# Optimization experiments

Measured on AMD Instinct MI355X. Metric: run time of the kernel, lower is better.

The kernel has to match this reference:

```python
import jax, jax.numpy as jnp
import numpy as np

IN_F = 512
OUT_F = 512
ALPHA = 0.2   # LeakyReLU negative slope
NEG_INF = -9e15


def setup_inputs() -> dict:
    key = jax.random.key(0)
    k1, k2, k3, k4 = jax.random.split(key, 4)
    B, S = 8, 2048
    hidden_state = jax.random.normal(k1, (B, S, IN_F), dtype=jnp.float32)
    adjacent_matrix = jax.random.uniform(k2, (B, S, S), dtype=jnp.float32)
    # nn.Linear weight (no bias): stored as [out, in] in torch; we keep [in, out] for x @ W
    bound = 1.0 / np.sqrt(IN_F)
    W = jax.random.uniform(k3, (IN_F, OUT_F), dtype=jnp.float32, minval=-bound, maxval=bound)
    # xavier_uniform with gain=1.414 on a: shape [2*out, 1]
    a_bound = 1.414 * np.sqrt(6.0 / (2 * OUT_F + 1))
    a = jax.random.uniform(k4, (2 * OUT_F, 1), dtype=jnp.float32, minval=-a_bound, maxval=a_bound)
    return {"hidden_state": hidden_state, "adjacent_matrix": adjacent_matrix, "W": W, "a": a}


def reference(hidden_state, adjacent_matrix, W, a):
    # Wh: [B, S, out]
    Wh = jnp.einsum('bsi,io->bso', hidden_state, W)
    # additive attention: Wh1 + Wh2^T -> [B, S, S]
    Wh1 = Wh @ a[:OUT_F, :]            # [B, S, 1]
    Wh2 = Wh @ a[OUT_F:, :]            # [B, S, 1]
    e = Wh1 + jnp.swapaxes(Wh2, 1, 2)  # [B, S, S]
    e = jax.nn.leaky_relu(e, negative_slope=ALPHA)
    attention = jnp.where(adjacent_matrix > 0.5, e, NEG_INF)
    # NOTE: original softmaxes over dim=1 (the *row* index), faithfully reproduced
    attention = jax.nn.softmax(attention, axis=1)
    # dropout is identity at inference (training=False)
    h_prime = jnp.einsum('bst,bto->bso', attention, Wh)
    return jax.nn.elu(h_prime)  # concat=True path
```

## Files before the change

### kernel.cpp

```cpp
#include <hip/hip_runtime.h>
#include <hip/hip_bf16.h>
#include <stdint.h>

#define SDIM 2048
#define BDIM 8
#define FDIM 512
constexpr float ALPHA = 0.2f;

typedef __attribute__((ext_vector_type(8))) short bf16x8;
typedef __attribute__((ext_vector_type(4))) float f32x4;

__device__ __forceinline__ unsigned short f2bf(float x) {
  __hip_bfloat16 h = __float2bfloat16(x);
  return *reinterpret_cast<unsigned short*>(&h);
}

__device__ __forceinline__ void gload_lds16(const void* g, void* l) {
  __builtin_amdgcn_global_load_lds(
      (const __attribute__((address_space(1))) unsigned int*)(uintptr_t)g,
      (__attribute__((address_space(3))) unsigned int*)(uintptr_t)l,
      16, 0, 0);
}

__global__ void k0_prep(const float* __restrict__ W, const float* __restrict__ a,
                        float* __restrict__ wa, __hip_bfloat16* __restrict__ WT) {
  int i = blockIdx.x;
  int lane = threadIdx.x;
  float s1 = 0.f, s2 = 0.f;
  for (int o = lane; o < FDIM; o += 64) {
    float w = W[i * FDIM + o];
    s1 += w * a[o];
    s2 += w * a[FDIM + o];
    WT[o * FDIM + i] = __float2bfloat16(w);
  }
  #pragma unroll
  for (int off = 32; off > 0; off >>= 1) {
    s1 += __shfl_down(s1, off);
    s2 += __shfl_down(s2, off);
  }
  if (lane == 0) { wa[i] = s1; wa[FDIM + i] = s2; }
}

__global__ __launch_bounds__(256) void k1_rows(const float* __restrict__ H,
                                               const float* __restrict__ wa,
                                               float* __restrict__ Wh1, float* __restrict__ Wh2,
                                               __hip_bfloat16* __restrict__ Hb) {
  int wid = threadIdx.x >> 6, lane = threadIdx.x & 63;
  long r = (long)blockIdx.x * 4 + wid;
  const float* hr = H + r * FDIM;
  float4 v0 = ((const float4*)hr)[lane];
  float4 v1 = ((const float4*)hr)[lane + 64];
  float4 wa10 = ((const float4*)wa)[lane];
  float4 wa11 = ((const float4*)wa)[lane + 64];
  float4 wa20 = ((const float4*)(wa + FDIM))[lane];
  float4 wa21 = ((const float4*)(wa + FDIM))[lane + 64];
  float s1 = v0.x*wa10.x + v0.y*wa10.y + v0.z*wa10.z + v0.w*wa10.w
           + v1.x*wa11.x + v1.y*wa11.y + v1.z*wa11.z + v1.w*wa11.w;
  float s2 = v0.x*wa20.x + v0.y*wa20.y + v0.z*wa20.z + v0.w*wa20.w
           + v1.x*wa21.x + v1.y*wa21.y + v1.z*wa21.z + v1.w*wa21.w;
  ushort4 u0 = { f2bf(v0.x), f2bf(v0.y), f2bf(v0.z), f2bf(v0.w) };
  ushort4 u1 = { f2bf(v1.x), f2bf(v1.y), f2bf(v1.z), f2bf(v1.w) };
  ushort4* hb = (ushort4*)(Hb + r * FDIM);
  hb[lane] = u0;
  hb[lane + 64] = u1;
  #pragma unroll
  for (int off = 32; off > 0; off >>= 1) {
    s1 += __shfl_down(s1, off);
    s2 += __shfl_down(s2, off);
  }
  if (lane == 0) { Wh1[r] = s1; Wh2[r] = s2; }
}

__global__ __launch_bounds__(256) void k2_z(const float* __restrict__ adj,
                                            const float* __restrict__ Wh1,
                                            const float* __restrict__ Wh2,
                                            float* __restrict__ Zp,
                                            __hip_bfloat16* __restrict__ P) {
  int t = blockIdx.x * 256 + threadIdx.x;
  int b = blockIdx.y;
  int c = blockIdx.z;
  float w2 = Wh2[b * SDIM + t];
  const float* arow = adj + ((long)b * SDIM + c * 64) * SDIM + t;
  const float* w1p = Wh1 + b * SDIM + c * 64;
  __hip_bfloat16* prow = P + ((long)b * SDIM + c * 64) * SDIM + t;
  float z = 0.f;
  #pragma unroll 8
  for (int s = 0; s < 64; ++s) {
    float av = arow[(long)s * SDIM];
    float e = w1p[s] + w2;
    e = fmaxf(e, ALPHA * e);
    float p = (av > 0.5f) ? __expf(e) : 0.f;
    z += p;
    prow[(long)s * SDIM] = __float2bfloat16(p);
  }
  Zp[(b * 32 + c) * SDIM + t] = z;
}

__global__ __launch_bounds__(256) void k3_gemm(const __hip_bfloat16* __restrict__ WTm,
                                               const __hip_bfloat16* __restrict__ Hb,
                                               const float* __restrict__ Zp,
                                               __hip_bfloat16* __restrict__ VT) {
  __shared__ __align__(16) __hip_bfloat16 Asm[2][128 * 32];
  __shared__ __align__(16) __hip_bfloat16 Bsm[2][128 * 32];
  __shared__ float ztmp[256];
  __shared__ float rzLds[128];
  const int o0 = blockIdx.x * 128;
  const int t0 = blockIdx.y * 128;
  const int b = blockIdx.z;
  const int tid = threadIdx.x;
  const int w = tid >> 6, lane = tid & 63;
  const int wm = w >> 1, wn = w & 1;
  const int fr = lane & 15, fq = lane >> 4;
  const int lr = lane >> 2, lb = (lane & 3) * 16;

  const __hip_bfloat16* Abase = WTm + (long)o0 * FDIM;
  const __hip_bfloat16* Bbase = Hb + ((long)b * SDIM + t0) * FDIM;

  f32x4 acc[4][4] = {};

  auto stage = [&](int kk, int buf) {
    #pragma unroll
    for (int g = 0; g < 2; ++g) {
      int rbase = g * 64 + w * 16;
      int row = rbase + lr;
      gload_lds16((const char*)(Abase + (long)row * FDIM + kk * 32) + lb,
                  (char*)&Asm[buf][0] + rbase * 64);
      gload_lds16((const char*)(Bbase + (long)row * FDIM + kk * 32) + lb,
                  (char*)&Bsm[buf][0] + rbase * 64);
    }
  };

  stage(0, 0);
  {
    int tl = tid & 127, h = tid >> 7;
    int t = t0 + tl;
    float z = 0.f;
    #pragma unroll
    for (int c = 0; c < 16; ++c)
      z += Zp[((b * 32) + h * 16 + c) * SDIM + t];
    ztmp[tid] = z;
  }
  __syncthreads();
  if (tid < 128) rzLds[tid] = 1.0f / (ztmp[tid] + ztmp[tid + 128]);
  __syncthreads();

  for (int kk = 0; kk < 16; ++kk) {
    int cur = kk & 1;
    if (kk < 15) stage(kk + 1, cur ^ 1);
    bf16x8 af[4], bf_[4];
    #pragma unroll
    for (int mf = 0; mf < 4; ++mf)
      af[mf] = *(const bf16x8*)((const char*)&Asm[cur][0] + (wm * 64 + mf * 16 + fr) * 64 + fq * 16);
    #pragma unroll
    for (int nf = 0; nf < 4; ++nf)
      bf_[nf] = *(const bf16x8*)((const char*)&Bsm[cur][0] + (wn * 64 + nf * 16 + fr) * 64 + fq * 16);
    #pragma unroll
    for (int mf = 0; mf < 4; ++mf)
      #pragma unroll
      for (int nf = 0; nf < 4; ++nf)
        acc[mf][nf] = __builtin_amdgcn_mfma_f32_16x16x32_bf16(af[mf], bf_[nf], acc[mf][nf], 0, 0, 0);
    __syncthreads();
  }

  #pragma unroll
  for (int nf = 0; nf < 4; ++nf) {
    int tl = wn * 64 + nf * 16 + fr;
    int t = t0 + tl;
    float rz = rzLds[tl];
    #pragma unroll
    for (int mf = 0; mf < 4; ++mf) {
      #pragma unroll
      for (int r = 0; r < 4; ++r) {
        int o = o0 + wm * 64 + mf * 16 + fq * 4 + r;
        VT[((long)(b * FDIM + o)) * SDIM + t] = __float2bfloat16(acc[mf][nf][r] * rz);
      }
    }
  }
}

__global__ __launch_bounds__(256, 2) void k4_pv(const __hip_bfloat16* __restrict__ P,
                                                const __hip_bfloat16* __restrict__ VT,
                                                float* __restrict__ out) {
  __shared__ __align__(16) __hip_bfloat16 Vsm[3][256 * 32];
  __shared__ __align__(16) __hip_bfloat16 Psm[3][64 * 32];
  const int b  = blockIdx.x;
  const int s0 = blockIdx.y * 64;
  const int ob = blockIdx.z * 256;
  const int tid = threadIdx.x;
  const int w = tid >> 6, lane = tid & 63;
  const int fr = lane & 15, fq = lane >> 4;
  const int srow = lane >> 2;
  const int sgam = (lane & 3) ^ ((lane >> 2) & 3);

  const char* vtG = (const char*)(VT + ((long)(b * FDIM + ob)) * SDIM);
  const char* pG  = (const char*)(P + ((long)(b * SDIM + s0)) * SDIM);

  f32x4 acc[4][4] = {};

  auto stageV = [&](int p, int buf) {
    #pragma unroll
    for (int g = 0; g < 4; ++g) {
      int row = w * 64 + g * 16 + srow;
      gload_lds16(vtG + ((long)row * SDIM + p * 32 + sgam * 8) * 2,
                  (char*)&Vsm[0][0] + buf * 16384 + w * 4096 + g * 1024);
    }
  };
  auto stageP = [&](int p, int buf) {
    int row = w * 16 + srow;
    gload_lds16(pG + ((long)row * SDIM + p * 32 + sgam * 8) * 2,
                (char*)&Psm[0][0] + buf * 4096 + w * 1024);
  };

  stageV(0, 0); stageP(0, 0);
  stageV(1, 1); stageP(1, 1);
  asm volatile("s_waitcnt vmcnt(5)" ::: "memory");
  __builtin_amdgcn_sched_barrier(0);
  __builtin_amdgcn_s_barrier();

  int bufR = 0;
  int bufS = 2;
  for (int p = 0; p < 64; ++p) {
    if (p <= 61) { stageV(p + 2, bufS); stageP(p + 2, bufS); }
    __builtin_amdgcn_sched_barrier(0);

    bf16x8 pa[4], vb[4];
    #pragma unroll
    for (int mf = 0; mf < 4; ++mf)
      pa[mf] = *(const bf16x8*)((const char*)&Psm[0][0] + bufR * 4096 + mf * 1024
                                + fr * 64 + (fq ^ (fr & 3)) * 16);
    #pragma unroll
    for (int nf = 0; nf < 4; ++nf)
      vb[nf] = *(const bf16x8*)((const char*)&Vsm[0][0] + bufR * 16384 + w * 4096 + nf * 1024
                                + fr * 64 + (fq ^ (fr & 3)) * 16);
    __builtin_amdgcn_s_setprio(1);
    #pragma unroll
    for (int mf = 0; mf < 4; ++mf)
      #pragma unroll
      for (int nf = 0; nf < 4; ++nf)
        acc[mf][nf] = __builtin_amdgcn_mfma_f32_16x16x32_bf16(pa[mf], vb[nf], acc[mf][nf], 0, 0, 0);
    __builtin_amdgcn_s_setprio(0);

    if (p <= 61) { asm volatile("s_waitcnt vmcnt(5)" ::: "memory"); }
    else         { asm volatile("s_waitcnt vmcnt(0)" ::: "memory"); }
    asm volatile("s_waitcnt lgkmcnt(0)" ::: "memory");
    __builtin_amdgcn_sched_barrier(0);
    __builtin_amdgcn_s_barrier();

    bufR = (bufR == 2) ? 0 : bufR + 1;
    bufS = (bufS == 2) ? 0 : bufS + 1;
  }

  float* orow = out + ((long)b * SDIM + s0) * FDIM + ob + w * 64;
  #pragma unroll
  for (int mf = 0; mf < 4; ++mf) {
    #pragma unroll
    for (int nf = 0; nf < 4; ++nf) {
      #pragma unroll
      for (int r = 0; r < 4; ++r) {
        int s = mf * 16 + fq * 4 + r;
        int o = nf * 16 + fr;
        float x = acc[mf][nf][r];
        x = x > 0.f ? x : (__expf(x) - 1.f);
        orow[(long)s * FDIM + o] = x;
      }
    }
  }
}

extern "C" void kernel_launch(void* const* d_in, const int* in_sizes, int n_in,
                              void* d_out, int out_size, void* d_ws, size_t ws_size,
                              hipStream_t stream) {
  const float* H   = (const float*)d_in[0];
  const float* adj = (const float*)d_in[1];
  const float* W   = (const float*)d_in[2];
  const float* a   = (const float*)d_in[3];
  float* out = (float*)d_out;
  char* ws = (char*)d_ws;

  __hip_bfloat16* VT  = (__hip_bfloat16*)(ws + 0);
  __hip_bfloat16* Hb  = (__hip_bfloat16*)(ws + 16777216);
  __hip_bfloat16* WT  = (__hip_bfloat16*)(ws + 33554432);
  float* wa  = (float*)(ws + 34078720);
  float* Wh1 = (float*)(ws + 34082816);
  float* Wh2 = (float*)(ws + 34148352);
  float* Zp  = (float*)(ws + 34279424);
  __hip_bfloat16* P = (__hip_bfloat16*)(ws + 37748736);

  hipLaunchKernelGGL(k0_prep, dim3(512), dim3(64), 0, stream, W, a, wa, WT);
  hipLaunchKernelGGL(k1_rows, dim3(4096), dim3(256), 0, stream, H, wa, Wh1, Wh2, Hb);
  hipLaunchKernelGGL(k2_z, dim3(8, 8, 32), dim3(256), 0, stream, adj, Wh1, Wh2, Zp, P);
  hipLaunchKernelGGL(k3_gemm, dim3(4, 16, 8), dim3(256), 0, stream, WT, Hb, Zp, VT);
  hipLaunchKernelGGL(k4_pv, dim3(8, 32, 2), dim3(256), 0, stream, P, VT, out);
}
```

Measured before the change: 120.8 us.

## Triple-buffer GEMM loads with vmcnt waits and tile the weight transpose

The k3 GEMM moves from a double-buffered to a triple-buffered LDS pipeline. Loads are issued two K-steps ahead, the full __syncthreads is replaced by explicit vmcnt/lgkmcnt waits plus s_barrier, and MFMA priority is raised with setprio. The k0 prep kernel now transposes W through a 64x64 shared-memory tile with coalesced packed bf16 stores, replacing strided scalar stores. The main risks are more LDS per block and correctness that depends on the hand-counted vmcnt values.

```diff
diff --git a/kernel.cpp b/kernel.cpp
--- a/kernel.cpp
+++ b/kernel.cpp
@@ -22,23 +22,62 @@
       16, 0, 0);
 }
 
-__global__ void k0_prep(const float* __restrict__ W, const float* __restrict__ a,
-                        float* __restrict__ wa, __hip_bfloat16* __restrict__ WT) {
-  int i = blockIdx.x;
-  int lane = threadIdx.x;
-  float s1 = 0.f, s2 = 0.f;
-  for (int o = lane; o < FDIM; o += 64) {
-    float w = W[i * FDIM + o];
-    s1 += w * a[o];
-    s2 += w * a[FDIM + o];
-    WT[o * FDIM + i] = __float2bfloat16(w);
-  }
-  #pragma unroll
-  for (int off = 32; off > 0; off >>= 1) {
-    s1 += __shfl_down(s1, off);
-    s2 += __shfl_down(s2, off);
-  }
-  if (lane == 0) { wa[i] = s1; wa[FDIM + i] = s2; }
+__global__ __launch_bounds__(256) void k0_prep(const float* __restrict__ W,
+                                               const float* __restrict__ a,
+                                               float* __restrict__ wa,
+                                               __hip_bfloat16* __restrict__ WT) {
+  __shared__ float tile[64][65];
+  const int bi = blockIdx.x, bo = blockIdx.y;
+  const int tid = threadIdx.x;
+  const int row = tid >> 2, quad = tid & 3;
+  const int i0 = bi * 64, o0 = bo * 64;
+
+  {
+    const float4* src = (const float4*)(W + (long)(i0 + row) * FDIM + o0 + quad * 16);
+    float4 v0 = src[0], v1 = src[1], v2 = src[2], v3 = src[3];
+    *(float4*)&tile[row][quad * 16 + 0]  = v0;
+    *(float4*)&tile[row][quad * 16 + 4]  = v1;
+    *(float4*)&tile[row][quad * 16 + 8]  = v2;
+    *(float4*)&tile[row][quad * 16 + 12] = v3;
+  }
+  __syncthreads();
+  {
+    bf16x8 pk0, pk1;
+    #pragma unroll
+    for (int j = 0; j < 8; ++j) pk0[j] = (short)f2bf(tile[quad * 16 + j][row]);
+    #pragma unroll
+    for (int j = 0; j < 8; ++j) pk1[j] = (short)f2bf(tile[quad * 16 + 8 + j][row]);
+    __hip_bfloat16* dst = WT + (long)(o0 + row) * FDIM + i0 + quad * 16;
+    *(bf16x8*)dst = pk0;
+    *(bf16x8*)(dst + 8) = pk1;
+  }
+
+  if (bo == 0) {
+    const int w = tid >> 6, lane = tid & 63;
+    float a1v[8], a2v[8];
+    #pragma unroll
+    for (int k = 0; k < 8; ++k) {
+      a1v[k] = a[lane + k * 64];
+      a2v[k] = a[FDIM + lane + k * 64];
+    }
+    for (int rr = 0; rr < 16; ++rr) {
+      int i = i0 + w * 16 + rr;
+      const float* wr = W + (long)i * FDIM;
+      float s1 = 0.f, s2 = 0.f;
+      #pragma unroll
+      for (int k = 0; k < 8; ++k) {
+        float x = wr[lane + k * 64];
+        s1 += x * a1v[k];
+        s2 += x * a2v[k];
+      }
+      #pragma unroll
+      for (int off = 32; off > 0; off >>= 1) {
+        s1 += __shfl_down(s1, off);
+        s2 += __shfl_down(s2, off);
+      }
+      if (lane == 0) { wa[i] = s1; wa[FDIM + i] = s2; }
+    }
+  }
 }
 
 __global__ __launch_bounds__(256) void k1_rows(const float* __restrict__ H,
@@ -96,12 +135,12 @@
   Zp[(b * 32 + c) * SDIM + t] = z;
 }
 
-__global__ __launch_bounds__(256) void k3_gemm(const __hip_bfloat16* __restrict__ WTm,
-                                               const __hip_bfloat16* __restrict__ Hb,
-                                               const float* __restrict__ Zp,
-                                               __hip_bfloat16* __restrict__ VT) {
-  __shared__ __align__(16) __hip_bfloat16 Asm[2][128 * 32];
-  __shared__ __align__(16) __hip_bfloat16 Bsm[2][128 * 32];
+__global__ __launch_bounds__(256, 2) void k3_gemm(const __hip_bfloat16* __restrict__ WTm,
+                                                  const __hip_bfloat16* __restrict__ Hb,
+                                                  const float* __restrict__ Zp,
+                                                  __hip_bfloat16* __restrict__ VT) {
+  __shared__ __align__(16) __hip_bfloat16 Asm[3][128 * 32];
+  __shared__ __align__(16) __hip_bfloat16 Bsm[3][128 * 32];
   __shared__ float ztmp[256];
   __shared__ float rzLds[128];
   const int o0 = blockIdx.x * 128;
@@ -124,13 +163,14 @@
       int rbase = g * 64 + w * 16;
       int row = rbase + lr;
       gload_lds16((const char*)(Abase + (long)row * FDIM + kk * 32) + lb,
-                  (char*)&Asm[buf][0] + rbase * 64);
+                  (char*)&Asm[0][0] + buf * 8192 + rbase * 64);
       gload_lds16((const char*)(Bbase + (long)row * FDIM + kk * 32) + lb,
-                  (char*)&Bsm[buf][0] + rbase * 64);
+                  (char*)&Bsm[0][0] + buf * 8192 + rbase * 64);
     }
   };
 
   stage(0, 0);
+  stage(1, 1);
   {
     int tl = tid & 127, h = tid >> 7;
     int t = t0 + tl;
@@ -140,26 +180,42 @@
       z += Zp[((b * 32) + h * 16 + c) * SDIM + t];
     ztmp[tid] = z;
   }
-  __syncthreads();
+  asm volatile("s_waitcnt lgkmcnt(0)" ::: "memory");
+  __builtin_amdgcn_sched_barrier(0);
+  __builtin_amdgcn_s_barrier();
   if (tid < 128) rzLds[tid] = 1.0f / (ztmp[tid] + ztmp[tid + 128]);
-  __syncthreads();
-
+  asm volatile("s_waitcnt vmcnt(4)" ::: "memory");
+  asm volatile("s_waitcnt lgkmcnt(0)" ::: "memory");
+  __builtin_amdgcn_sched_barrier(0);
+  __builtin_amdgcn_s_barrier();
+
+  int bufR = 0, bufS = 2;
   for (int kk = 0; kk < 16; ++kk) {
-    int cur = kk & 1;
-    if (kk < 15) stage(kk + 1, cur ^ 1);
+    if (kk <= 13) stage(kk + 2, bufS);
+    __builtin_amdgcn_sched_barrier(0);
     bf16x8 af[4], bf_[4];
     #pragma unroll
     for (int mf = 0; mf < 4; ++mf)
-      af[mf] = *(const bf16x8*)((const char*)&Asm[cur][0] + (wm * 64 + mf * 16 + fr) * 64 + fq * 16);
+      af[mf] = *(const bf16x8*)((const char*)&Asm[0][0] + bufR * 8192
+                                + (wm * 64 + mf * 16 + fr) * 64 + fq * 16);
     #pragma unroll
     for (int nf = 0; nf < 4; ++nf)
-      bf_[nf] = *(const bf16x8*)((const char*)&Bsm[cur][0] + (wn * 64 + nf * 16 + fr) * 64 + fq * 16);
+      bf_[nf] = *(const bf16x8*)((const char*)&Bsm[0][0] + bufR * 8192
+                                 + (wn * 64 + nf * 16 + fr) * 64 + fq * 16);
+    __builtin_amdgcn_s_setprio(1);
     #pragma unroll
     for (int mf = 0; mf < 4; ++mf)
       #pragma unroll
       for (int nf = 0; nf < 4; ++nf)
         acc[mf][nf] = __builtin_amdgcn_mfma_f32_16x16x32_bf16(af[mf], bf_[nf], acc[mf][nf], 0, 0, 0);
-    __syncthreads();
+    __builtin_amdgcn_s_setprio(0);
+    if (kk <= 13) { asm volatile("s_waitcnt vmcnt(4)" ::: "memory"); }
+    else          { asm volatile("s_waitcnt vmcnt(0)" ::: "memory"); }
+    asm volatile("s_waitcnt lgkmcnt(0)" ::: "memory");
+    __builtin_amdgcn_sched_barrier(0);
+    __builtin_amdgcn_s_barrier();
+    bufR = (bufR == 2) ? 0 : bufR + 1;
+    bufS = (bufS == 2) ? 0 : bufS + 1;
   }
 
   #pragma unroll
@@ -286,7 +342,7 @@
   float* Zp  = (float*)(ws + 34279424);
   __hip_bfloat16* P = (__hip_bfloat16*)(ws + 37748736);
 
-  hipLaunchKernelGGL(k0_prep, dim3(512), dim3(64), 0, stream, W, a, wa, WT);
+  hipLaunchKernelGGL(k0_prep, dim3(8, 8), dim3(256), 0, stream, W, a, wa, WT);
   hipLaunchKernelGGL(k1_rows, dim3(4096), dim3(256), 0, stream, H, wa, Wh1, Wh2, Hb);
   hipLaunchKernelGGL(k2_z, dim3(8, 8, 32), dim3(256), 0, stream, adj, Wh1, Wh2, Zp, P);
   hipLaunchKernelGGL(k3_gemm, dim3(4, 16, 8), dim3(256), 0, stream, WT, Hb, Zp, VT);
```

Result: slower. 124.2 us (+2.8%).
